# Kernel optimization log

Hardware: AMD Instinct MI355X
Metric: run time of the kernel (lower is better)

The kernel has to match this reference:

```python
import jax, jax.numpy as jnp
import numpy as np

NEG = -10000.0

def _wn(W, g):
    # weight_norm with dim=None: single scalar g scaling W / ||W||_F
    return g * W / jnp.linalg.norm(W)

def setup_inputs() -> dict:
    key = jax.random.key(0)
    ks = jax.random.split(key, 10)
    B, N, H, P = 128, 4096, 128, 128
    v = jax.random.normal(ks[0], (B, N, H), jnp.float32)
    q = jax.random.normal(ks[1], (B, H), jnp.float32)
    mask = jnp.ones((B, N), jnp.float32)
    # params (out_dim, in_dim) like torch Linear
    Wv = jax.random.normal(ks[2], (P, H), jnp.float32) / np.sqrt(H)
    bv = jnp.zeros((P,), jnp.float32)
    gv = jnp.float32(jnp.linalg.norm(Wv))
    Wq = jax.random.normal(ks[3], (P, H), jnp.float32) / np.sqrt(H)
    bq = jnp.zeros((P,), jnp.float32)
    gq = jnp.float32(jnp.linalg.norm(Wq))
    Wa = jax.random.normal(ks[4], (1, P), jnp.float32) / np.sqrt(P)
    ba = jnp.zeros((1,), jnp.float32)
    ga = jnp.float32(jnp.linalg.norm(Wa))
    return {"v": v, "q": q, "mask": mask, "Wv": Wv, "bv": bv, "gv": gv,
            "Wq": Wq, "bq": bq, "gq": gq, "Wa": Wa, "ba": ba, "ga": ga}

def reference(v, q, mask, Wv, bv, gv, Wq, bq, gq, Wa, ba, ga):
    # FCNet projections (dropout is identity at inference; FCNet applies no relu)
    v_proj = jnp.einsum('bnh,ph->bnp', v, _wn(Wv, gv)) + bv        # [B,N,P]
    q_proj = (q @ _wn(Wq, gq).T + bq)[:, None, :]                   # [B,1,P]
    h = jax.nn.relu(v_proj + q_proj)                                # [B,N,P]
    logits = jnp.einsum('bnp,p->bn', h, _wn(Wa, ga)[0]) + ba[0]     # [B,N]
    logits = logits + (1.0 - mask) * NEG
    w = jax.nn.softmax(logits, axis=-1)                             # [B,N]
    w_att = w[:, :, None]                                           # [B,N,1]
    att = jnp.sum(v * w_att, axis=1)                                # [B,H]
    return att, w_att
```

## Files before the change

kernel.cpp:

```cpp
#include <hip/hip_runtime.h>

typedef _Float16 half8_t __attribute__((ext_vector_type(8)));
typedef float f32x4 __attribute__((ext_vector_type(4)));

#define B_ 128
#define N_ 4096
#define H_ 128
#define P_ 128
#define CCH 8
#define ROWS_PER_CHUNK (N_ / CCH)
#define TILES (ROWS_PER_CHUNK / 64)

#define OFF_SCALES 0
#define OFF_WA     16
#define OFF_BPACK  16640
#define OFF_LOGITS 24832
#define OFF_PART   549120

__global__ __launch_bounds__(1024) void k0_prep(
    const float* __restrict__ Wv, const float* __restrict__ gv,
    const float* __restrict__ Wq, const float* __restrict__ gq,
    const float* __restrict__ Wa, const float* __restrict__ ga,
    float* __restrict__ ws)
{
    const int tid  = threadIdx.x;
    const int lane = tid & 63;
    const int w    = tid >> 6;

    float sv2 = 0.f, sq2 = 0.f, sa2 = 0.f;
    const float4* Wv4 = (const float4*)Wv;
    const float4* Wq4 = (const float4*)Wq;
#pragma unroll
    for (int i = 0; i < 4; ++i) {
        float4 a = Wv4[tid + i * 1024];
        sv2 += a.x * a.x + a.y * a.y + a.z * a.z + a.w * a.w;
        float4 b = Wq4[tid + i * 1024];
        sq2 += b.x * b.x + b.y * b.y + b.z * b.z + b.w * b.w;
    }
    if (tid < P_) { float z = Wa[tid]; sa2 = z * z; }

#pragma unroll
    for (int m = 1; m <= 32; m <<= 1) {
        sv2 += __shfl_xor(sv2, m, 64);
        sq2 += __shfl_xor(sq2, m, 64);
        sa2 += __shfl_xor(sa2, m, 64);
    }
    __shared__ float rv[16], rq[16], ra[16];
    __shared__ float s_sv, s_sa;
    if (lane == 0) { rv[w] = sv2; rq[w] = sq2; ra[w] = sa2; }
    __syncthreads();
    if (tid == 0) {
        float nv = 0.f, nq = 0.f, na = 0.f;
#pragma unroll
        for (int i = 0; i < 16; ++i) { nv += rv[i]; nq += rq[i]; na += ra[i]; }
        float sv = gv[0] / sqrtf(nv);
        float sq = gq[0] / sqrtf(nq);
        float sa = ga[0] / sqrtf(na);
        ws[OFF_SCALES + 0] = sv;
        ws[OFF_SCALES + 1] = sq;
        ws[OFF_SCALES + 2] = sa;
        s_sv = sv; s_sa = sa;
    }
    __syncthreads();

    const float sv = s_sv, sa = s_sa;
    _Float16* bp = (_Float16*)(ws + OFF_BPACK);
#pragma unroll
    for (int k = 0; k < 16; ++k) {
        int s  = tid + k * 1024;
        int j  = s & 7;
        int L  = (s >> 3) & 63;
        int pt = (s >> 9) & 7;
        int kk = s >> 12;
        int p = pt * 16 + (L & 15);
        int h = kk * 32 + (L >> 4) * 8 + j;
        bp[s] = (_Float16)(Wv[p * H_ + h] * sv);
    }
    if (tid < P_) ws[OFF_WA + tid] = Wa[tid] * sa;
}

__global__ __launch_bounds__(256) void k1_main(
    const float* __restrict__ v, const float* __restrict__ mask,
    const float* __restrict__ ba,
    const float* __restrict__ q, const float* __restrict__ Wq,
    const float* __restrict__ bq, const float* __restrict__ bv,
    float* __restrict__ ws)
{
    const int c = blockIdx.x;
    const int b = blockIdx.y;
    const int tid = threadIdx.x;
    const int lane = tid & 63;
    const int w = tid >> 6;

    __shared__ __align__(16) _Float16 Bl[16384];
    __shared__ float qpcs[P_];
    __shared__ float was[P_];
    __shared__ float smask[ROWS_PER_CHUNK];
    __shared__ float obuf[4][P_];
    __shared__ float mbuf[4], lbuf[4];

    {
        const uint4* src = (const uint4*)(ws + OFF_BPACK);
        uint4* dst = (uint4*)Bl;
#pragma unroll
        for (int i = 0; i < 8; ++i) dst[tid + i * 256] = src[tid + i * 256];

        const int p  = tid >> 1;
        const int hh = tid & 1;
        const float sq = ws[OFF_SCALES + 1];
        const float4* qr = (const float4*)(q + (size_t)b * H_) + hh * 16;
        const float4* wr = (const float4*)(Wq + (size_t)p * H_) + hh * 16;
        float acc = 0.f;
#pragma unroll
        for (int i = 0; i < 16; ++i) {
            float4 a = qr[i], cc4 = wr[i];
            acc += a.x * cc4.x + a.y * cc4.y + a.z * cc4.z + a.w * cc4.w;
        }
        acc += __shfl_xor(acc, 1, 64);
        if (hh == 0) qpcs[p] = acc * sq + bq[p] + bv[p];

        if (tid < P_) was[tid] = ws[OFF_WA + tid];
#pragma unroll
        for (int i = 0; i < ROWS_PER_CHUNK / 256; ++i)
            smask[tid + i * 256] = mask[(size_t)b * N_ + c * ROWS_PER_CHUNK + tid + i * 256];
    }
    const float ba0 = ba[0];
    __syncthreads();

    const int rloc = lane & 15;
    const int grp  = lane >> 4;
    const int colb = grp * 8;

    float m_w = -1e30f, l_w = 0.f;
    float o32[32];
#pragma unroll
    for (int j = 0; j < 32; ++j) o32[j] = 0.f;

    for (int it = 0; it < TILES; ++it) {
        const int r0 = it * 64 + w * 16;
        const int n0w = c * ROWS_PER_CHUNK + r0;

        const float* vrow = v + ((size_t)b * N_ + n0w + rloc) * H_;
        half8_t af[4];
#pragma unroll
        for (int kk = 0; kk < 4; ++kk) {
            const float4* p4 = (const float4*)(vrow + kk * 32 + colb);
            float4 f0 = p4[0], f1 = p4[1];
            half8_t a;
            a[0] = (_Float16)f0.x; a[1] = (_Float16)f0.y;
            a[2] = (_Float16)f0.z; a[3] = (_Float16)f0.w;
            a[4] = (_Float16)f1.x; a[5] = (_Float16)f1.y;
            a[6] = (_Float16)f1.z; a[7] = (_Float16)f1.w;
            af[kk] = a;
        }

        float lp[4];
        lp[0] = lp[1] = lp[2] = lp[3] = 0.f;
#pragma unroll
        for (int pt = 0; pt < 8; ++pt) {
            const int p = pt * 16 + rloc;
            const float qv = qpcs[p];
            f32x4 acc = {qv, qv, qv, qv};
#pragma unroll
            for (int kk = 0; kk < 4; ++kk) {
                half8_t bf = *(const half8_t*)&Bl[(((kk * 8 + pt) * 64) + lane) * 8];
                acc = __builtin_amdgcn_mfma_f32_16x16x32_f16(af[kk], bf, acc, 0, 0, 0);
            }
            const float wv = was[p];
#pragma unroll
            for (int r = 0; r < 4; ++r)
                lp[r] += fmaxf(acc[r], 0.f) * wv;
        }
#pragma unroll
        for (int m = 1; m <= 8; m <<= 1) {
#pragma unroll
            for (int r = 0; r < 4; ++r) lp[r] += __shfl_xor(lp[r], m, 64);
        }
#pragma unroll
        for (int r = 0; r < 4; ++r) {
            const float mk = smask[r0 + grp * 4 + r];
            lp[r] += ba0 + (1.0f - mk) * (-10000.0f);
        }

        const int srcl = (rloc >> 2) << 4;
        float t0 = __shfl(lp[0], srcl, 64);
        float t1 = __shfl(lp[1], srcl, 64);
        float t2 = __shfl(lp[2], srcl, 64);
        float t3 = __shfl(lp[3], srcl, 64);
        float a01 = (rloc & 1) ? t1 : t0;
        float a23 = (rloc & 1) ? t3 : t2;
        float lg_me = (rloc & 2) ? a23 : a01;

        if (lane < 16) ws[OFF_LOGITS + (size_t)b * N_ + n0w + lane] = lg_me;

        float mt = fmaxf(fmaxf(lp[0], lp[1]), fmaxf(lp[2], lp[3]));
        mt = fmaxf(mt, __shfl_xor(mt, 16, 64));
        mt = fmaxf(mt, __shfl_xor(mt, 32, 64));

        const float mn = fmaxf(m_w, mt);
        const float alpha = __expf(m_w - mn);
        const float wme = __expf(lg_me - mn);
        float s = wme;
#pragma unroll
        for (int m = 1; m <= 8; m <<= 1) s += __shfl_xor(s, m, 64);
        l_w = l_w * alpha + s;
        m_w = mn;

        if (alpha != 1.0f) {
#pragma unroll
            for (int j = 0; j < 32; ++j) o32[j] *= alpha;
        }
#pragma unroll
        for (int kk = 0; kk < 4; ++kk) {
#pragma unroll
            for (int j = 0; j < 8; ++j)
                o32[kk * 8 + j] += wme * (float)af[kk][j];
        }
    }

#pragma unroll
    for (int m = 1; m <= 8; m <<= 1) {
#pragma unroll
        for (int j = 0; j < 32; ++j) o32[j] += __shfl_xor(o32[j], m, 64);
    }
    {
        const int j0 = rloc * 2;
#pragma unroll
        for (int u = 0; u < 2; ++u) {
            const int j = j0 + u;
            obuf[w][(j >> 3) * 32 + colb + (j & 7)] = o32[j];
        }
        if (lane == 0) { mbuf[w] = m_w; lbuf[w] = l_w; }
    }
    __syncthreads();

    float* part = ws + OFF_PART + ((size_t)b * CCH + c) * 132;
    if (tid < P_) {
        const float mb = fmaxf(fmaxf(mbuf[0], mbuf[1]), fmaxf(mbuf[2], mbuf[3]));
        float lb = 0.f, oh = 0.f;
#pragma unroll
        for (int ww = 0; ww < 4; ++ww) {
            const float e = __expf(mbuf[ww] - mb);
            lb += e * lbuf[ww];
            oh += e * obuf[ww][tid];
        }
        part[2 + tid] = oh;
        if (tid == 0) { part[0] = mb; part[1] = lb; }
    }
}

__global__ __launch_bounds__(256) void k2_final(
    const float* __restrict__ ws, float* __restrict__ out)
{
    const int c4 = blockIdx.x;
    const int b  = blockIdx.y;
    const int tid = threadIdx.x;
    const float* part = ws + OFF_PART + (size_t)b * CCH * 132;

    float m = -1e30f;
#pragma unroll
    for (int cc = 0; cc < CCH; ++cc) m = fmaxf(m, part[cc * 132]);
    float l = 0.f;
#pragma unroll
    for (int cc = 0; cc < CCH; ++cc)
        l += __expf(part[cc * 132] - m) * part[cc * 132 + 1];
    const float il = 1.0f / l;

    if (c4 == 0 && tid < P_) {
        float a = 0.f;
#pragma unroll
        for (int cc = 0; cc < CCH; ++cc)
            a += __expf(part[cc * 132] - m) * part[cc * 132 + 2 + tid];
        out[(size_t)b * H_ + tid] = a * il;
    }

    const float4* lg4 = (const float4*)(ws + OFF_LOGITS + (size_t)b * N_ + c4 * 1024);
    float4* w4 = (float4*)(out + B_ * H_ + (size_t)b * N_ + c4 * 1024);
    float4 g = lg4[tid];
    float4 r;
    r.x = __expf(g.x - m) * il;
    r.y = __expf(g.y - m) * il;
    r.z = __expf(g.z - m) * il;
    r.w = __expf(g.w - m) * il;
    w4[tid] = r;
}

extern "C" void kernel_launch(void* const* d_in, const int* in_sizes, int n_in,
                              void* d_out, int out_size, void* d_ws, size_t ws_size,
                              hipStream_t stream) {
    const float* v    = (const float*)d_in[0];
    const float* q    = (const float*)d_in[1];
    const float* mask = (const float*)d_in[2];
    const float* Wv   = (const float*)d_in[3];
    const float* bv   = (const float*)d_in[4];
    const float* gv   = (const float*)d_in[5];
    const float* Wq   = (const float*)d_in[6];
    const float* bq   = (const float*)d_in[7];
    const float* gq   = (const float*)d_in[8];
    const float* Wa   = (const float*)d_in[9];
    const float* ba   = (const float*)d_in[10];
    const float* ga   = (const float*)d_in[11];
    float* out = (float*)d_out;
    float* ws  = (float*)d_ws;

    k0_prep<<<1, 1024, 0, stream>>>(Wv, gv, Wq, gq, Wa, ga, ws);
    k1_main<<<dim3(CCH, B_), 256, 0, stream>>>(v, mask, ba, q, Wq, bq, bv, ws);
    k2_final<<<dim3(4, B_), 256, 0, stream>>>(ws, out);
}
```

Baseline: 407.3 us.

## Fuse prep and finalize kernels into main kernel via last-block atomic counter

Removes the separate weight-prep kernel: each block now computes the weight-norm scales and packs Wv into fp16 LDS itself, with the Wv scale folded into the q-projection and Wa instead of into the packed weights. The final softmax-combine kernel is also folded in. The last block to finish for each batch row, detected with an atomic counter that a memset zeroes on every call, merges the partials and writes the normalized weights. This saves kernel launches and the prep-kernel serialization, at the cost of redundant per-block norm reductions, a memset launch, and a serialized tail handled by one block per row.

```diff
diff --git a/kernel.cpp b/kernel.cpp
--- a/kernel.cpp
+++ b/kernel.cpp
@@ -11,80 +11,19 @@
 #define ROWS_PER_CHUNK (N_ / CCH)
 #define TILES (ROWS_PER_CHUNK / 64)
 
-#define OFF_SCALES 0
-#define OFF_WA     16
-#define OFF_BPACK  16640
+#define OFF_CNT    1024
 #define OFF_LOGITS 24832
 #define OFF_PART   549120
 
-__global__ __launch_bounds__(1024) void k0_prep(
-    const float* __restrict__ Wv, const float* __restrict__ gv,
-    const float* __restrict__ Wq, const float* __restrict__ gq,
-    const float* __restrict__ Wa, const float* __restrict__ ga,
-    float* __restrict__ ws)
-{
-    const int tid  = threadIdx.x;
-    const int lane = tid & 63;
-    const int w    = tid >> 6;
-
-    float sv2 = 0.f, sq2 = 0.f, sa2 = 0.f;
-    const float4* Wv4 = (const float4*)Wv;
-    const float4* Wq4 = (const float4*)Wq;
-#pragma unroll
-    for (int i = 0; i < 4; ++i) {
-        float4 a = Wv4[tid + i * 1024];
-        sv2 += a.x * a.x + a.y * a.y + a.z * a.z + a.w * a.w;
-        float4 b = Wq4[tid + i * 1024];
-        sq2 += b.x * b.x + b.y * b.y + b.z * b.z + b.w * b.w;
-    }
-    if (tid < P_) { float z = Wa[tid]; sa2 = z * z; }
-
-#pragma unroll
-    for (int m = 1; m <= 32; m <<= 1) {
-        sv2 += __shfl_xor(sv2, m, 64);
-        sq2 += __shfl_xor(sq2, m, 64);
-        sa2 += __shfl_xor(sa2, m, 64);
-    }
-    __shared__ float rv[16], rq[16], ra[16];
-    __shared__ float s_sv, s_sa;
-    if (lane == 0) { rv[w] = sv2; rq[w] = sq2; ra[w] = sa2; }
-    __syncthreads();
-    if (tid == 0) {
-        float nv = 0.f, nq = 0.f, na = 0.f;
-#pragma unroll
-        for (int i = 0; i < 16; ++i) { nv += rv[i]; nq += rq[i]; na += ra[i]; }
-        float sv = gv[0] / sqrtf(nv);
-        float sq = gq[0] / sqrtf(nq);
-        float sa = ga[0] / sqrtf(na);
-        ws[OFF_SCALES + 0] = sv;
-        ws[OFF_SCALES + 1] = sq;
-        ws[OFF_SCALES + 2] = sa;
-        s_sv = sv; s_sa = sa;
-    }
-    __syncthreads();
-
-    const float sv = s_sv, sa = s_sa;
-    _Float16* bp = (_Float16*)(ws + OFF_BPACK);
-#pragma unroll
-    for (int k = 0; k < 16; ++k) {
-        int s  = tid + k * 1024;
-        int j  = s & 7;
-        int L  = (s >> 3) & 63;
-        int pt = (s >> 9) & 7;
-        int kk = s >> 12;
-        int p = pt * 16 + (L & 15);
-        int h = kk * 32 + (L >> 4) * 8 + j;
-        bp[s] = (_Float16)(Wv[p * H_ + h] * sv);
-    }
-    if (tid < P_) ws[OFF_WA + tid] = Wa[tid] * sa;
-}
-
-__global__ __launch_bounds__(256) void k1_main(
+__global__ __launch_bounds__(256) void k_fused(
     const float* __restrict__ v, const float* __restrict__ mask,
     const float* __restrict__ ba,
     const float* __restrict__ q, const float* __restrict__ Wq,
     const float* __restrict__ bq, const float* __restrict__ bv,
-    float* __restrict__ ws)
+    const float* __restrict__ Wv, const float* __restrict__ gv,
+    const float* __restrict__ gq, const float* __restrict__ Wa,
+    const float* __restrict__ ga,
+    float* __restrict__ ws, float* __restrict__ out)
 {
     const int c = blockIdx.x;
     const int b = blockIdx.y;
@@ -98,31 +37,72 @@
     __shared__ float smask[ROWS_PER_CHUNK];
     __shared__ float obuf[4][P_];
     __shared__ float mbuf[4], lbuf[4];
+    __shared__ float red3[4][3];
+    __shared__ int s_win;
+
+    float sv2 = 0.f, sq2 = 0.f, sa2 = 0.f;
+
+#pragma unroll
+    for (int g = 0; g < 8; ++g) {
+        const int idx = w * 8 + g;
+        const int kk = idx >> 3, pt = idx & 7;
+        const int p = pt * 16 + (lane & 15);
+        const int h = kk * 32 + (lane >> 4) * 8;
+        const float4* src = (const float4*)(Wv + (size_t)p * H_ + h);
+        float4 f0 = src[0], f1 = src[1];
+        sv2 += f0.x * f0.x + f0.y * f0.y + f0.z * f0.z + f0.w * f0.w
+             + f1.x * f1.x + f1.y * f1.y + f1.z * f1.z + f1.w * f1.w;
+        half8_t a;
+        a[0] = (_Float16)f0.x; a[1] = (_Float16)f0.y;
+        a[2] = (_Float16)f0.z; a[3] = (_Float16)f0.w;
+        a[4] = (_Float16)f1.x; a[5] = (_Float16)f1.y;
+        a[6] = (_Float16)f1.z; a[7] = (_Float16)f1.w;
+        *(half8_t*)&Bl[(((kk * 8 + pt) * 64) + lane) * 8] = a;
+    }
 
     {
-        const uint4* src = (const uint4*)(ws + OFF_BPACK);
-        uint4* dst = (uint4*)Bl;
-#pragma unroll
-        for (int i = 0; i < 8; ++i) dst[tid + i * 256] = src[tid + i * 256];
-
         const int p  = tid >> 1;
         const int hh = tid & 1;
-        const float sq = ws[OFF_SCALES + 1];
         const float4* qr = (const float4*)(q + (size_t)b * H_) + hh * 16;
         const float4* wr = (const float4*)(Wq + (size_t)p * H_) + hh * 16;
-        float acc = 0.f;
+        float dot = 0.f;
 #pragma unroll
         for (int i = 0; i < 16; ++i) {
-            float4 a = qr[i], cc4 = wr[i];
-            acc += a.x * cc4.x + a.y * cc4.y + a.z * cc4.z + a.w * cc4.w;
-        }
-        acc += __shfl_xor(acc, 1, 64);
-        if (hh == 0) qpcs[p] = acc * sq + bq[p] + bv[p];
-
-        if (tid < P_) was[tid] = ws[OFF_WA + tid];
-#pragma unroll
-        for (int i = 0; i < ROWS_PER_CHUNK / 256; ++i)
-            smask[tid + i * 256] = mask[(size_t)b * N_ + c * ROWS_PER_CHUNK + tid + i * 256];
+            float4 a = qr[i], c4 = wr[i];
+            dot += a.x * c4.x + a.y * c4.y + a.z * c4.z + a.w * c4.w;
+            sq2 += c4.x * c4.x + c4.y * c4.y + c4.z * c4.z + c4.w * c4.w;
+        }
+        dot += __shfl_xor(dot, 1, 64);
+        if (hh == 0) qpcs[p] = dot;
+    }
+
+    float wa_z = 0.f;
+    if (tid < P_) { wa_z = Wa[tid]; sa2 = wa_z * wa_z; }
+
+#pragma unroll
+    for (int i = 0; i < ROWS_PER_CHUNK / 256; ++i)
+        smask[tid + i * 256] = mask[(size_t)b * N_ + c * ROWS_PER_CHUNK + tid + i * 256];
+
+#pragma unroll
+    for (int m = 1; m <= 32; m <<= 1) {
+        sv2 += __shfl_xor(sv2, m, 64);
+        sq2 += __shfl_xor(sq2, m, 64);
+        sa2 += __shfl_xor(sa2, m, 64);
+    }
+    if (lane == 0) { red3[w][0] = sv2; red3[w][1] = sq2; red3[w][2] = sa2; }
+    __syncthreads();
+    const float nv = red3[0][0] + red3[1][0] + red3[2][0] + red3[3][0];
+    const float nq = red3[0][1] + red3[1][1] + red3[2][1] + red3[3][1];
+    const float na = red3[0][2] + red3[1][2] + red3[2][2] + red3[3][2];
+    const float rnv = sqrtf(nv);
+    const float sv = gv[0] / rnv;
+    const float inv_sv = rnv / gv[0];
+    const float sq = gq[0] / sqrtf(nq);
+    const float sa = ga[0] / sqrtf(na);
+
+    if (tid < P_) {
+        qpcs[tid] = (qpcs[tid] * sq + bq[tid] + bv[tid]) * inv_sv;
+        was[tid]  = wa_z * (sa * sv);
     }
     const float ba0 = ba[0];
     __syncthreads();
@@ -234,29 +214,33 @@
     }
     __syncthreads();
 
-    float* part = ws + OFF_PART + ((size_t)b * CCH + c) * 132;
-    if (tid < P_) {
-        const float mb = fmaxf(fmaxf(mbuf[0], mbuf[1]), fmaxf(mbuf[2], mbuf[3]));
-        float lb = 0.f, oh = 0.f;
-#pragma unroll
-        for (int ww = 0; ww < 4; ++ww) {
-            const float e = __expf(mbuf[ww] - mb);
-            lb += e * lbuf[ww];
-            oh += e * obuf[ww][tid];
-        }
-        part[2 + tid] = oh;
-        if (tid == 0) { part[0] = mb; part[1] = lb; }
-    }
-}
-
-__global__ __launch_bounds__(256) void k2_final(
-    const float* __restrict__ ws, float* __restrict__ out)
-{
-    const int c4 = blockIdx.x;
-    const int b  = blockIdx.y;
-    const int tid = threadIdx.x;
+    {
+        float* part = ws + OFF_PART + ((size_t)b * CCH + c) * 132;
+        if (tid < P_) {
+            const float mb = fmaxf(fmaxf(mbuf[0], mbuf[1]), fmaxf(mbuf[2], mbuf[3]));
+            float lb = 0.f, oh = 0.f;
+#pragma unroll
+            for (int ww = 0; ww < 4; ++ww) {
+                const float e = __expf(mbuf[ww] - mb);
+                lb += e * lbuf[ww];
+                oh += e * obuf[ww][tid];
+            }
+            part[2 + tid] = oh;
+            if (tid == 0) { part[0] = mb; part[1] = lb; }
+        }
+    }
+
+    __syncthreads();
+    if (tid == 0) {
+        __threadfence();
+        int old = atomicAdd((int*)ws + OFF_CNT + b, 1);
+        s_win = (old == CCH - 1) ? 1 : 0;
+    }
+    __syncthreads();
+    if (!s_win) return;
+    __threadfence();
+
     const float* part = ws + OFF_PART + (size_t)b * CCH * 132;
-
     float m = -1e30f;
 #pragma unroll
     for (int cc = 0; cc < CCH; ++cc) m = fmaxf(m, part[cc * 132]);
@@ -266,7 +250,7 @@
         l += __expf(part[cc * 132] - m) * part[cc * 132 + 1];
     const float il = 1.0f / l;
 
-    if (c4 == 0 && tid < P_) {
+    if (tid < P_) {
         float a = 0.f;
 #pragma unroll
         for (int cc = 0; cc < CCH; ++cc)
@@ -274,15 +258,19 @@
         out[(size_t)b * H_ + tid] = a * il;
     }
 
-    const float4* lg4 = (const float4*)(ws + OFF_LOGITS + (size_t)b * N_ + c4 * 1024);
-    float4* w4 = (float4*)(out + B_ * H_ + (size_t)b * N_ + c4 * 1024);
-    float4 g = lg4[tid];
-    float4 r;
-    r.x = __expf(g.x - m) * il;
-    r.y = __expf(g.y - m) * il;
-    r.z = __expf(g.z - m) * il;
-    r.w = __expf(g.w - m) * il;
-    w4[tid] = r;
+    const float4* lg4 = (const float4*)(ws + OFF_LOGITS + (size_t)b * N_);
+    float4* w4 = (float4*)(out + B_ * H_ + (size_t)b * N_);
+#pragma unroll
+    for (int u = 0; u < 4; ++u) {
+        const int i = tid + u * 256;
+        float4 g = lg4[i];
+        float4 r;
+        r.x = __expf(g.x - m) * il;
+        r.y = __expf(g.y - m) * il;
+        r.z = __expf(g.z - m) * il;
+        r.w = __expf(g.w - m) * il;
+        w4[i] = r;
+    }
 }
 
 extern "C" void kernel_launch(void* const* d_in, const int* in_sizes, int n_in,
@@ -303,7 +291,7 @@
     float* out = (float*)d_out;
     float* ws  = (float*)d_ws;
 
-    k0_prep<<<1, 1024, 0, stream>>>(Wv, gv, Wq, gq, Wa, ga, ws);
-    k1_main<<<dim3(CCH, B_), 256, 0, stream>>>(v, mask, ba, q, Wq, bq, bv, ws);
-    k2_final<<<dim3(4, B_), 256, 0, stream>>>(ws, out);
+    hipMemsetAsync((char*)d_ws + OFF_CNT * sizeof(int), 0, B_ * sizeof(int), stream);
+    k_fused<<<dim3(CCH, B_), 256, 0, stream>>>(v, mask, ba, q, Wq, bq, bv,
+                                               Wv, gv, gq, Wa, ga, ws, out);
 }
```

New measurement: 517.3 us. +27.0%, slower.
